# Performance work log

Hardware: AMD Instinct MI355X
Metric: run time of the kernel (lower is better)

The kernel has to match this reference:

```python
import jax, jax.numpy as jnp
import numpy as np

C = 256  # channels
B, H, W = 16, 64, 64


def _conv1x1(x, w, b):
    # x: [B,Cin,H,W], w: [Cout,Cin], b: [Cout] -> [B,Cout,H,W]
    return jnp.einsum('bchw,oc->bohw', x, w) + b[None, :, None, None]


def _axis_attn(x, wq, bq, wf, bf, axis):
    # axis: -1 for 'W', -2 for 'H'
    qkv = _conv1x1(x, wq, bq)                      # [B,1+2C,H,W]
    query = qkv[:, :1]                             # [B,1,H,W]
    key = qkv[:, 1:1 + C]                          # [B,C,H,W]
    value = qkv[:, 1 + C:]                         # [B,C,H,W]
    scores = jax.nn.softmax(query, axis=axis)      # softmax over spatial axis
    context = jnp.sum(key * scores, axis=axis, keepdims=True)  # [B,C,H,1] or [B,C,1,W]
    gate = jax.nn.sigmoid(value)
    out = x + gate * context                       # broadcast over reduced axis
    return _conv1x1(out, wf, bf)


def setup_inputs() -> dict:
    key = jax.random.key(0)
    ks = jax.random.split(key, 5)
    s_qkv = 1.0 / np.sqrt(C)
    s_fus = 1.0 / np.sqrt(C)
    return {
        'x': jax.random.normal(ks[0], (B, C, H, W), dtype=jnp.float32),
        'qkvW_w': jax.random.normal(ks[1], (1 + 2 * C, C), dtype=jnp.float32) * s_qkv,
        'qkvW_b': jnp.zeros((1 + 2 * C,), dtype=jnp.float32),
        'qkvH_w': jax.random.normal(ks[2], (1 + 2 * C, C), dtype=jnp.float32) * s_qkv,
        'qkvH_b': jnp.zeros((1 + 2 * C,), dtype=jnp.float32),
        'fusW_w': jax.random.normal(ks[3], (C, C), dtype=jnp.float32) * s_fus,
        'fusW_b': jnp.zeros((C,), dtype=jnp.float32),
        'fusH_w': jax.random.normal(ks[4], (C, C), dtype=jnp.float32) * s_fus,
        'fusH_b': jnp.zeros((C,), dtype=jnp.float32),
    }


def reference(x, qkvW_w, qkvW_b, qkvH_w, qkvH_b, fusW_w, fusW_b, fusH_w, fusH_b):
    x_w = _axis_attn(x, qkvW_w, qkvW_b, fusW_w, fusW_b, axis=-1)
    x_h = _axis_attn(x_w, qkvH_w, qkvH_b, fusH_w, fusH_b, axis=-2)
    return x_h
```

## Files before the change

kernel.cpp:

```cpp
#include <hip/hip_runtime.h>

typedef unsigned short u16;
typedef unsigned int u32;
typedef __attribute__((ext_vector_type(8))) short bf16x8;
typedef __attribute__((ext_vector_type(4))) float f32x4;

__device__ __forceinline__ u16 f2bf(float f) {
    u32 u = __builtin_bit_cast(u32, f);
    u += 0x7FFFu + ((u >> 16) & 1u);
    return (u16)(u >> 16);
}
__device__ __forceinline__ float bf2f(u16 s) {
    u32 u = ((u32)s) << 16;
    return __builtin_bit_cast(float, u);
}
__device__ __forceinline__ float sigm(float x) {
    return 1.0f / (1.0f + __expf(-x));
}
__device__ __forceinline__ void gload16(const u16* g, u16* l) {
    __builtin_amdgcn_global_load_lds(
        (const __attribute__((address_space(1))) void*)g,
        (__attribute__((address_space(3))) void*)l, 16, 0, 0);
}

__global__ __launch_bounds__(256) void transpose_in(const float* __restrict__ x,
                                                    u16* __restrict__ xp) {
    __shared__ float tile[64][65];
    int bid = blockIdx.x;
    int ct = bid & 3, h = (bid >> 2) & 63, b = bid >> 8;
    int t = threadIdx.x;
    int tr = t >> 4, tc = t & 15;
    const float* src = x + (((size_t)(b * 256 + ct * 64) * 64 + h) * 64);
#pragma unroll
    for (int i = 0; i < 4; ++i) {
        int c = tr + i * 16;
        float4 v = *(const float4*)(src + (size_t)c * 4096 + tc * 4);
        tile[c][tc * 4 + 0] = v.x;
        tile[c][tc * 4 + 1] = v.y;
        tile[c][tc * 4 + 2] = v.z;
        tile[c][tc * 4 + 3] = v.w;
    }
    __syncthreads();
    u16* dst = xp + ((size_t)((b * 64 + h) * 64)) * 256 + ct * 64;
#pragma unroll
    for (int i = 0; i < 4; ++i) {
        int w = tr + i * 16;
        ushort4 o;
        o.x = f2bf(tile[tc * 4 + 0][w]);
        o.y = f2bf(tile[tc * 4 + 1][w]);
        o.z = f2bf(tile[tc * 4 + 2][w]);
        o.w = f2bf(tile[tc * 4 + 3][w]);
        *(ushort4*)(dst + (size_t)w * 256 + tc * 4) = o;
    }
}

__global__ __launch_bounds__(256) void prep_w(const float* __restrict__ qw,
                                              const float* __restrict__ qb,
                                              const float* __restrict__ fw,
                                              const float* __restrict__ fb,
                                              float* __restrict__ wq0,
                                              u16* __restrict__ wkv,
                                              float* __restrict__ bkv,
                                              u16* __restrict__ wf,
                                              float* __restrict__ bff) {
    int i = blockIdx.x * 256 + threadIdx.x;
    if (i < 513 * 256) {
        int o = i >> 8, c = i & 255;
        float v = qw[i];
        if (o == 0) wq0[c] = v;
        else        wkv[(size_t)(o - 1) * 256 + c] = f2bf(v);
    }
    if (i < 65536) wf[i] = f2bf(fw[i]);
    if (i < 512)   bkv[i] = qb[i + 1];
    if (i < 256)   bff[i] = fb[i];
}

template <int AXIS>
__global__ __launch_bounds__(256) void line_ctx(
    const u16* __restrict__ A, const u16* __restrict__ Wk,
    const float* __restrict__ wq0, const float* __restrict__ bkv,
    float* __restrict__ ctx) {
    __shared__ alignas(16) u16 Xl[64 * 256];
    __shared__ float ql[64];
    __shared__ float sc[64];
    __shared__ alignas(16) float ys[256];
    int t = threadIdx.x, lane = t & 63, wv = t >> 6;
    int l = blockIdx.x;
    auto prow = [&](int r) -> size_t {
        if (AXIS == 0) return (size_t)l * 64 + r;
        else           return (size_t)(l >> 6) * 4096 + (size_t)r * 64 + (l & 63);
    };
#pragma unroll
    for (int i = 0; i < 8; ++i) {
        int row = i * 8 + wv * 2 + (lane >> 5);
        int slot = (lane & 31) ^ (row & 7);
        gload16(A + prow(row) * 256 + slot * 8, &Xl[(i * 8 + wv * 2) * 256]);
    }
    __syncthreads();
    {
        int row = t >> 2, g = t & 3;
        const float* wp = wq0 + g * 64;
        float a = 0.f;
#pragma unroll
        for (int cc = 0; cc < 8; ++cc) {
            int slot = (g * 8 + cc) ^ (row & 7);
            bf16x8 v = *(const bf16x8*)&Xl[row * 256 + slot * 8];
#pragma unroll
            for (int j = 0; j < 8; ++j) a += bf2f((u16)v[j]) * wp[cc * 8 + j];
        }
        a += __shfl_xor(a, 1);
        a += __shfl_xor(a, 2);
        if (g == 0) ql[row] = a;
    }
    __syncthreads();
    if (t < 64) {
        float qv = ql[t];
        float m = qv;
#pragma unroll
        for (int off = 32; off > 0; off >>= 1) m = fmaxf(m, __shfl_xor(m, off));
        float e = __expf(qv - m);
        float s = e;
#pragma unroll
        for (int off = 32; off > 0; off >>= 1) s += __shfl_xor(s, off);
        sc[t] = e / s;
    }
    __syncthreads();
    {
        int chunk = t >> 3, e7 = t & 7;
        float a = 0.f;
#pragma unroll 8
        for (int p = 0; p < 64; ++p) {
            int slot = chunk ^ (p & 7);
            a += bf2f(Xl[p * 256 + slot * 8 + e7]) * sc[p];
        }
        ys[t] = a;
    }
    __syncthreads();
    {
        const u16* wk = Wk + (size_t)t * 256;
        float a = 0.f;
#pragma unroll
        for (int kc = 0; kc < 32; ++kc) {
            bf16x8 w = *(const bf16x8*)(wk + kc * 8);
#pragma unroll
            for (int j = 0; j < 8; ++j) a += bf2f((u16)w[j]) * ys[kc * 8 + j];
        }
        ctx[(size_t)l * 256 + t] = a + bkv[t];
    }
}

template <int AXIS>
__global__ __launch_bounds__(256, 2) void val_gate(
    const u16* __restrict__ A, const u16* __restrict__ Wv,
    const float* __restrict__ bv, const float* __restrict__ ctx,
    u16* __restrict__ G) {
    int h = blockIdx.x;
    int xcd = h & 7, slot = h >> 3;
    int otile = slot & 1, ptile = xcd * 64 + (slot >> 1);
    __shared__ alignas(16) u16 Asm[128 * 64];
    __shared__ alignas(16) u16 Bsm[128 * 64];
    __shared__ alignas(16) float ctxs[2][128];
    int o0 = otile * 128;
    int t = threadIdx.x, lane = t & 63, wv = t >> 6;
    int arow = lane & 15, kgrp = lane >> 4, l7 = lane & 7;
    int rowhalf = wv & 1, chhalf = wv >> 1;
    auto prow = [&](int r) -> size_t {
        if (AXIS == 0) return (size_t)ptile * 128 + r;
        else           return (size_t)(ptile >> 5) * 4096 + (size_t)(r & 63) * 64 +
                              ((ptile & 31) * 2) + (r >> 6);
    };
    int lbase = (AXIS == 0) ? (ptile * 2) : ((ptile >> 5) * 64 + (ptile & 31) * 2);
    {
        int ll = t >> 7, cl = t & 127;
        ctxs[ll][cl] = ctx[(size_t)(lbase + ll) * 256 + o0 + cl];
    }
    f32x4 zero = {0.f, 0.f, 0.f, 0.f};
    f32x4 acc[4][4];
#pragma unroll
    for (int i = 0; i < 4; ++i)
#pragma unroll
        for (int jj = 0; jj < 4; ++jj) acc[i][jj] = zero;

    for (int k0 = 0; k0 < 256; k0 += 64) {
        __syncthreads();
#pragma unroll
        for (int it = 0; it < 4; ++it) {
            int r0 = it * 32 + wv * 8;
            int rr = r0 + (lane >> 3);
            int chs = ((l7 ^ (lane >> 3)) * 8);
            gload16(A + prow(rr) * 256 + k0 + chs, &Asm[r0 * 64]);
            gload16(Wv + (size_t)(o0 + rr) * 256 + k0 + chs, &Bsm[r0 * 64]);
        }
        __syncthreads();
#pragma unroll
        for (int kk = 0; kk < 64; kk += 32) {
            int soff = (((kk >> 3) + kgrp) ^ l7) << 3;
            bf16x8 xf[4], wf[4];
#pragma unroll
            for (int xi = 0; xi < 4; ++xi)
                xf[xi] = *(const bf16x8*)&Asm[(rowhalf * 64 + xi * 16 + arow) * 64 + soff];
#pragma unroll
            for (int wi = 0; wi < 4; ++wi)
                wf[wi] = *(const bf16x8*)&Bsm[(chhalf * 64 + wi * 16 + arow) * 64 + soff];
#pragma unroll
            for (int wi = 0; wi < 4; ++wi)
#pragma unroll
                for (int xi = 0; xi < 4; ++xi)
                    acc[wi][xi] = __builtin_amdgcn_mfma_f32_16x16x32_bf16(
                        wf[wi], xf[xi], acc[wi][xi], 0, 0, 0);
        }
    }
#pragma unroll
    for (int wi = 0; wi < 4; ++wi) {
        int chl = chhalf * 64 + wi * 16 + kgrp * 4;
        int ch = o0 + chl;
        f32x4 bq = *(const f32x4*)&bv[ch];
        f32x4 cx = *(const f32x4*)&ctxs[rowhalf][chl];
#pragma unroll
        for (int xi = 0; xi < 4; ++xi) {
            int row = rowhalf * 64 + xi * 16 + arow;
            size_t p = prow(row);
            ushort4 xv = *(const ushort4*)(A + p * 256 + ch);
            ushort4 o;
            o.x = f2bf(bf2f(xv.x) + sigm(acc[wi][xi][0] + bq[0]) * cx[0]);
            o.y = f2bf(bf2f(xv.y) + sigm(acc[wi][xi][1] + bq[1]) * cx[1]);
            o.z = f2bf(bf2f(xv.z) + sigm(acc[wi][xi][2] + bq[2]) * cx[2]);
            o.w = f2bf(bf2f(xv.w) + sigm(acc[wi][xi][3] + bq[3]) * cx[3]);
            *(ushort4*)(G + p * 256 + ch) = o;
        }
    }
}

template <int MODE>
__global__ __launch_bounds__(256, 2) void gemm_k(
    const u16* __restrict__ A, const u16* __restrict__ Bw,
    const float* __restrict__ bias,
    u16* __restrict__ bOut, float* __restrict__ fOut) {
    int h = blockIdx.x;
    int xcd = h & 7, slot = h >> 3;
    int otile = slot & 1, ptile = xcd * 64 + (slot >> 1);
    __shared__ alignas(16) u16 Asm[128 * 64];
    __shared__ alignas(16) u16 Bsm[128 * 64];
    __shared__ alignas(16) float tb[(MODE == 2) ? 64 * 132 : 4];
    int p0 = ptile * 128, o0 = otile * 128;
    int t = threadIdx.x, lane = t & 63, wv = t >> 6;
    int wm = (wv >> 1) * 64, wn = (wv & 1) * 64;
    int l7 = lane & 7;
    int srcoff = (lane >> 3) * 256 + (((lane & 7) ^ (lane >> 3)) * 8);
    int arow = lane & 15, kgrp = lane >> 4;
    f32x4 zero = {0.f, 0.f, 0.f, 0.f};
    f32x4 acc[4][4];
#pragma unroll
    for (int i = 0; i < 4; ++i)
#pragma unroll
        for (int jj = 0; jj < 4; ++jj) acc[i][jj] = zero;

    for (int k0 = 0; k0 < 256; k0 += 64) {
        __syncthreads();
#pragma unroll
        for (int it = 0; it < 4; ++it) {
            int r0 = it * 32 + wv * 8;
            gload16(A + (size_t)(p0 + r0) * 256 + k0 + srcoff, &Asm[r0 * 64]);
            gload16(Bw + (size_t)(o0 + r0) * 256 + k0 + srcoff, &Bsm[r0 * 64]);
        }
        __syncthreads();
#pragma unroll
        for (int kk = 0; kk < 64; kk += 32) {
            int soff = (((kk >> 3) + kgrp) ^ l7) << 3;
            bf16x8 af[4], bfv[4];
#pragma unroll
            for (int mi = 0; mi < 4; ++mi)
                af[mi] = *(const bf16x8*)&Asm[(wm + mi * 16 + arow) * 64 + soff];
#pragma unroll
            for (int ni = 0; ni < 4; ++ni)
                bfv[ni] = *(const bf16x8*)&Bsm[(wn + ni * 16 + arow) * 64 + soff];
            if (MODE == 1) {
#pragma unroll
                for (int ni = 0; ni < 4; ++ni)
#pragma unroll
                    for (int mi = 0; mi < 4; ++mi)
                        acc[ni][mi] = __builtin_amdgcn_mfma_f32_16x16x32_bf16(
                            bfv[ni], af[mi], acc[ni][mi], 0, 0, 0);
            } else {
#pragma unroll
                for (int mi = 0; mi < 4; ++mi)
#pragma unroll
                    for (int ni = 0; ni < 4; ++ni)
                        acc[mi][ni] = __builtin_amdgcn_mfma_f32_16x16x32_bf16(
                            af[mi], bfv[ni], acc[mi][ni], 0, 0, 0);
            }
        }
    }
    if (MODE == 1) {
#pragma unroll
        for (int ni = 0; ni < 4; ++ni) {
            int col0 = o0 + wn + ni * 16 + kgrp * 4;
            f32x4 bq = *(const f32x4*)&bias[col0];
#pragma unroll
            for (int mi = 0; mi < 4; ++mi) {
                int row = p0 + wm + mi * 16 + arow;
                ushort4 o;
                o.x = f2bf(acc[ni][mi][0] + bq[0]);
                o.y = f2bf(acc[ni][mi][1] + bq[1]);
                o.z = f2bf(acc[ni][mi][2] + bq[2]);
                o.w = f2bf(acc[ni][mi][3] + bq[3]);
                *(ushort4*)(bOut + (size_t)row * 256 + col0) = o;
            }
        }
    } else {
        int bb = p0 >> 12, pl = p0 & 4095;
#pragma unroll
        for (int cp = 0; cp < 2; ++cp) {
            if ((wv & 1) == cp) {
#pragma unroll
                for (int ni = 0; ni < 4; ++ni) {
                    int c = ni * 16 + arow;
                    float bvv = bias[o0 + cp * 64 + c];
#pragma unroll
                    for (int mi = 0; mi < 4; ++mi) {
                        int r0w = wm + mi * 16 + kgrp * 4;
                        f32x4 v;
                        v[0] = acc[mi][ni][0] + bvv;
                        v[1] = acc[mi][ni][1] + bvv;
                        v[2] = acc[mi][ni][2] + bvv;
                        v[3] = acc[mi][ni][3] + bvv;
                        *(f32x4*)&tb[c * 132 + r0w] = v;
                    }
                }
            }
            __syncthreads();
#pragma unroll
            for (int i = 0; i < 8; ++i) {
                int c = i * 8 + (t >> 5);
                f32x4 v = *(const f32x4*)&tb[c * 132 + (t & 31) * 4];
                *(float4*)&fOut[(size_t)(bb * 256 + o0 + cp * 64 + c) * 4096 +
                                pl + (t & 31) * 4] = *(float4*)&v;
            }
            if (cp == 0) __syncthreads();
        }
    }
}

extern "C" void kernel_launch(void* const* d_in, const int* in_sizes, int n_in,
                              void* d_out, int out_size, void* d_ws, size_t ws_size,
                              hipStream_t stream) {
    const float* x   = (const float*)d_in[0];
    const float* qWw = (const float*)d_in[1];
    const float* qWb = (const float*)d_in[2];
    const float* qHw = (const float*)d_in[3];
    const float* qHb = (const float*)d_in[4];
    const float* fWw = (const float*)d_in[5];
    const float* fWb = (const float*)d_in[6];
    const float* fHw = (const float*)d_in[7];
    const float* fHb = (const float*)d_in[8];
    float* out = (float*)d_out;

    char* ws = (char*)d_ws;
    size_t off = 0;
    auto carve = [&](size_t bytes) -> void* {
        off = (off + 255) & ~(size_t)255;
        void* p = ws + off;
        off += bytes;
        return p;
    };
    const size_t P = 65536;
    u16*   xp  = (u16*)carve(P * 256 * 2);
    u16*   kb  = (u16*)carve(P * 256 * 2);
    u16*   vb  = (u16*)carve(P * 256 * 2);
    float* ctxb = (float*)carve(1024 * 256 * 4);
    float* wq01 = (float*)carve(256 * 4);
    u16*   wkv1 = (u16*)carve(512 * 256 * 2);
    float* bkv1 = (float*)carve(512 * 4);
    u16*   wf1  = (u16*)carve(65536 * 2);
    float* bf1  = (float*)carve(256 * 4);
    float* wq02 = (float*)carve(256 * 4);
    u16*   wkv2 = (u16*)carve(512 * 256 * 2);
    float* bkv2 = (float*)carve(512 * 4);
    u16*   wf2  = (u16*)carve(65536 * 2);
    float* bf2  = (float*)carve(256 * 4);

    prep_w<<<513, 256, 0, stream>>>(qWw, qWb, fWw, fWb, wq01, wkv1, bkv1, wf1, bf1);
    prep_w<<<513, 256, 0, stream>>>(qHw, qHb, fHw, fHb, wq02, wkv2, bkv2, wf2, bf2);
    transpose_in<<<4096, 256, 0, stream>>>(x, xp);

    line_ctx<0><<<1024, 256, 0, stream>>>(xp, wkv1, wq01, bkv1, ctxb);
    val_gate<0><<<1024, 256, 0, stream>>>(xp, wkv1 + 256 * 256, bkv1 + 256,
                                          ctxb, kb);
    gemm_k<1><<<1024, 256, 0, stream>>>(kb, wf1, bf1, vb, nullptr);
    line_ctx<1><<<1024, 256, 0, stream>>>(vb, wkv2, wq02, bkv2, ctxb);
    val_gate<1><<<1024, 256, 0, stream>>>(vb, wkv2 + 256 * 256, bkv2 + 256,
                                          ctxb, kb);
    gemm_k<2><<<1024, 256, 0, stream>>>(kb, wf2, bf2, nullptr, out);
    (void)in_sizes; (void)n_in; (void)out_size; (void)ws_size;
}
```

Baseline: 178.4 us.

## Stage full-K activation tile in LDS for val_gate and write fp32 output directly

val_gate now loads the whole 128x256 activation tile into LDS once, with an XOR swizzle. That tile feeds every K step of the MFMA and also supplies the residual x values in the epilogue, replacing per-k reloads and a second global read. The ctx and bias values move from shared memory into per-thread registers. Separately, the MODE 2 GEMM epilogue drops the LDS transpose buffer and its syncs and writes f32x4 directly to the channel-major output. The larger LDS footprint (64KB+16KB) may lower occupancy, and the direct stores are less coalesced.

```diff
diff --git a/kernel.cpp b/kernel.cpp
--- a/kernel.cpp
+++ b/kernel.cpp
@@ -154,26 +154,38 @@
     const u16* __restrict__ A, const u16* __restrict__ Wv,
     const float* __restrict__ bv, const float* __restrict__ ctx,
     u16* __restrict__ G) {
+    __shared__ alignas(16) u16 Asm[128 * 256];
+    __shared__ alignas(16) u16 Bsm[128 * 64];
     int h = blockIdx.x;
     int xcd = h & 7, slot = h >> 3;
     int otile = slot & 1, ptile = xcd * 64 + (slot >> 1);
-    __shared__ alignas(16) u16 Asm[128 * 64];
-    __shared__ alignas(16) u16 Bsm[128 * 64];
-    __shared__ alignas(16) float ctxs[2][128];
     int o0 = otile * 128;
     int t = threadIdx.x, lane = t & 63, wv = t >> 6;
     int arow = lane & 15, kgrp = lane >> 4, l7 = lane & 7;
-    int rowhalf = wv & 1, chhalf = wv >> 1;
+    int wm = (wv >> 1) * 64, wn = (wv & 1) * 64;
     auto prow = [&](int r) -> size_t {
         if (AXIS == 0) return (size_t)ptile * 128 + r;
         else           return (size_t)(ptile >> 5) * 4096 + (size_t)(r & 63) * 64 +
                               ((ptile & 31) * 2) + (r >> 6);
     };
     int lbase = (AXIS == 0) ? (ptile * 2) : ((ptile >> 5) * 64 + (ptile & 31) * 2);
+    f32x4 cxr[4], bvr[4];
     {
-        int ll = t >> 7, cl = t & 127;
-        ctxs[ll][cl] = ctx[(size_t)(lbase + ll) * 256 + o0 + cl];
-    }
+        int line = lbase + (wv >> 1);
+#pragma unroll
+        for (int wi = 0; wi < 4; ++wi) {
+            int ch = o0 + wn + wi * 16 + kgrp * 4;
+            cxr[wi] = *(const f32x4*)&ctx[(size_t)line * 256 + ch];
+            bvr[wi] = *(const f32x4*)&bv[ch];
+        }
+    }
+#pragma unroll
+    for (int i = 0; i < 16; ++i) {
+        int row = i * 8 + wv * 2 + (lane >> 5);
+        int slotc = (lane & 31) ^ (row & 7);
+        gload16(A + prow(row) * 256 + slotc * 8, &Asm[(i * 8 + wv * 2) * 256]);
+    }
+    int srcoff = (lane >> 3) * 256 + (((lane & 7) ^ (lane >> 3)) * 8);
     f32x4 zero = {0.f, 0.f, 0.f, 0.f};
     f32x4 acc[4][4];
 #pragma unroll
@@ -186,10 +198,7 @@
 #pragma unroll
         for (int it = 0; it < 4; ++it) {
             int r0 = it * 32 + wv * 8;
-            int rr = r0 + (lane >> 3);
-            int chs = ((l7 ^ (lane >> 3)) * 8);
-            gload16(A + prow(rr) * 256 + k0 + chs, &Asm[r0 * 64]);
-            gload16(Wv + (size_t)(o0 + rr) * 256 + k0 + chs, &Bsm[r0 * 64]);
+            gload16(Wv + (size_t)(o0 + r0) * 256 + k0 + srcoff, &Bsm[r0 * 64]);
         }
         __syncthreads();
 #pragma unroll
@@ -197,11 +206,15 @@
             int soff = (((kk >> 3) + kgrp) ^ l7) << 3;
             bf16x8 xf[4], wf[4];
 #pragma unroll
-            for (int xi = 0; xi < 4; ++xi)
-                xf[xi] = *(const bf16x8*)&Asm[(rowhalf * 64 + xi * 16 + arow) * 64 + soff];
+            for (int xi = 0; xi < 4; ++xi) {
+                int p = wm + xi * 16 + arow;
+                int chunk = ((k0 + kk) >> 3) + kgrp;
+                int slt = chunk ^ (p & 7);
+                xf[xi] = *(const bf16x8*)&Asm[p * 256 + slt * 8];
+            }
 #pragma unroll
             for (int wi = 0; wi < 4; ++wi)
-                wf[wi] = *(const bf16x8*)&Bsm[(chhalf * 64 + wi * 16 + arow) * 64 + soff];
+                wf[wi] = *(const bf16x8*)&Bsm[(wn + wi * 16 + arow) * 64 + soff];
 #pragma unroll
             for (int wi = 0; wi < 4; ++wi)
 #pragma unroll
@@ -212,21 +225,21 @@
     }
 #pragma unroll
     for (int wi = 0; wi < 4; ++wi) {
-        int chl = chhalf * 64 + wi * 16 + kgrp * 4;
+        int chl = wn + wi * 16 + kgrp * 4;
         int ch = o0 + chl;
-        f32x4 bq = *(const f32x4*)&bv[ch];
-        f32x4 cx = *(const f32x4*)&ctxs[rowhalf][chl];
+        f32x4 bq = bvr[wi];
+        f32x4 cx = cxr[wi];
 #pragma unroll
         for (int xi = 0; xi < 4; ++xi) {
-            int row = rowhalf * 64 + xi * 16 + arow;
-            size_t p = prow(row);
-            ushort4 xv = *(const ushort4*)(A + p * 256 + ch);
+            int p = wm + xi * 16 + arow;
+            int slt = (ch >> 3) ^ (p & 7);
+            ushort4 xv = *(const ushort4*)&Asm[p * 256 + slt * 8 + (ch & 7)];
             ushort4 o;
             o.x = f2bf(bf2f(xv.x) + sigm(acc[wi][xi][0] + bq[0]) * cx[0]);
             o.y = f2bf(bf2f(xv.y) + sigm(acc[wi][xi][1] + bq[1]) * cx[1]);
             o.z = f2bf(bf2f(xv.z) + sigm(acc[wi][xi][2] + bq[2]) * cx[2]);
             o.w = f2bf(bf2f(xv.w) + sigm(acc[wi][xi][3] + bq[3]) * cx[3]);
-            *(ushort4*)(G + p * 256 + ch) = o;
+            *(ushort4*)(G + prow(p) * 256 + ch) = o;
         }
     }
 }
@@ -241,7 +254,6 @@
     int otile = slot & 1, ptile = xcd * 64 + (slot >> 1);
     __shared__ alignas(16) u16 Asm[128 * 64];
     __shared__ alignas(16) u16 Bsm[128 * 64];
-    __shared__ alignas(16) float tb[(MODE == 2) ? 64 * 132 : 4];
     int p0 = ptile * 128, o0 = otile * 128;
     int t = threadIdx.x, lane = t & 63, wv = t >> 6;
     int wm = (wv >> 1) * 64, wn = (wv & 1) * 64;
@@ -308,35 +320,18 @@
             }
         }
     } else {
-        int bb = p0 >> 12, pl = p0 & 4095;
-#pragma unroll
-        for (int cp = 0; cp < 2; ++cp) {
-            if ((wv & 1) == cp) {
-#pragma unroll
-                for (int ni = 0; ni < 4; ++ni) {
-                    int c = ni * 16 + arow;
-                    float bvv = bias[o0 + cp * 64 + c];
-#pragma unroll
-                    for (int mi = 0; mi < 4; ++mi) {
-                        int r0w = wm + mi * 16 + kgrp * 4;
-                        f32x4 v;
-                        v[0] = acc[mi][ni][0] + bvv;
-                        v[1] = acc[mi][ni][1] + bvv;
-                        v[2] = acc[mi][ni][2] + bvv;
-                        v[3] = acc[mi][ni][3] + bvv;
-                        *(f32x4*)&tb[c * 132 + r0w] = v;
-                    }
-                }
+        int bb = p0 >> 12;
+#pragma unroll
+        for (int mi = 0; mi < 4; ++mi) {
+            int row0 = p0 + wm + mi * 16 + kgrp * 4;
+#pragma unroll
+            for (int ni = 0; ni < 4; ++ni) {
+                int col = o0 + wn + ni * 16 + arow;
+                float bvv = bias[col];
+                f32x4 v = acc[mi][ni];
+                v[0] += bvv; v[1] += bvv; v[2] += bvv; v[3] += bvv;
+                *(f32x4*)&fOut[((size_t)(bb * 256 + col)) * 4096 + (row0 & 4095)] = v;
             }
-            __syncthreads();
-#pragma unroll
-            for (int i = 0; i < 8; ++i) {
-                int c = i * 8 + (t >> 5);
-                f32x4 v = *(const f32x4*)&tb[c * 132 + (t & 31) * 4];
-                *(float4*)&fOut[(size_t)(bb * 256 + o0 + cp * 64 + c) * 4096 +
-                                pl + (t & 31) * 4] = *(float4*)&v;
-            }
-            if (cp == 0) __syncthreads();
         }
     }
 }
```

Result: faster. 174.6 us (-2.2%).
